# Optimization experiments

Measured on AMD Instinct MI355X. Metric: run time of the kernel, lower is better.

Reference implementation:

```python
import jax, jax.numpy as jnp
import numpy as np

B, S, HID = 2, 2048, 1024
H, KV, D = 8, 4, 128
GROUPS = H // KV
SCALE = D ** -0.5
ROPE_THETA = 10000.0


def _rope_tables(seq_len, dim):
    inv = 1.0 / (ROPE_THETA ** (jnp.arange(0, dim, 2, dtype=jnp.float32) / dim))
    t = jnp.arange(seq_len, dtype=jnp.float32)
    freqs = jnp.outer(t, inv)                          # [S, D/2]
    emb = jnp.concatenate([freqs, freqs], axis=-1)     # [S, D]
    return jnp.cos(emb), jnp.sin(emb)


def _rotate_half(x):
    x1, x2 = jnp.split(x, 2, axis=-1)
    return jnp.concatenate([-x2, x1], axis=-1)


def setup_inputs() -> dict:
    key = jax.random.key(0)
    ks = jax.random.split(key, 7)
    std = 0.02
    hidden = jax.random.normal(ks[0], (B, S, HID), jnp.float32)
    Wq = jax.random.normal(ks[1], (HID, H * D), jnp.float32) * std
    Wk = jax.random.normal(ks[2], (HID, KV * D), jnp.float32) * std
    Wv = jax.random.normal(ks[3], (HID, KV * D), jnp.float32) * std
    Wdt = jax.random.normal(ks[4], (KV * D, H), jnp.float32) * std
    A = jax.random.normal(ks[5], (H,), jnp.float32) * 0.1
    Wo = jax.random.normal(ks[6], (H * D, HID), jnp.float32) * std
    cos, sin = _rope_tables(S, D)
    causal_mask = jnp.triu(jnp.ones((S, S), jnp.int32), 1)[None, None]  # 1 = masked
    return dict(hidden=hidden, Wq=Wq, Wk=Wk, Wv=Wv, Wdt=Wdt, A=A, Wo=Wo,
                cos=cos, sin=sin, causal_mask=causal_mask)


def reference(hidden, Wq, Wk, Wv, Wdt, A, Wo, cos, sin, causal_mask):
    # q/k/v projections -> [B, heads, S, D]
    q = (hidden @ Wq).reshape(B, S, H, D).transpose(0, 2, 1, 3)
    k = (hidden @ Wk).reshape(B, S, KV, D).transpose(0, 2, 1, 3)
    v = (hidden @ Wv).reshape(B, S, KV, D).transpose(0, 2, 1, 3)
    # RoPE
    c = cos[None, None]  # [1,1,S,D]
    s = sin[None, None]
    q = q * c + _rotate_half(q) * s
    k = k * c + _rotate_half(k) * s
    # dynamic mask: dt_proj over flattened per-position value states
    v_flat = v.transpose(0, 2, 1, 3).reshape(B, S, KV * D)
    dt = v_flat @ Wdt                                        # [B, S, H]
    dyn = jnp.exp(A[None, None, :] * jax.nn.softplus(dt))    # [B, S, H]
    attn_bias = dyn.transpose(0, 2, 1)[:, :, None, :]        # [B, H, 1, kv]
    min_val = jnp.finfo(jnp.float32).min
    attn_bias = jnp.where(causal_mask != 0, min_val, attn_bias)  # [B, H, S, S]
    # GQA repeat of kv heads
    k_rep = jnp.repeat(k, GROUPS, axis=1)
    v_rep = jnp.repeat(v, GROUPS, axis=1)
    scores = jnp.einsum('bhqd,bhkd->bhqk', q, k_rep) * SCALE + attn_bias
    w = jax.nn.softmax(scores.astype(jnp.float32), axis=-1).astype(hidden.dtype)
    out = jnp.einsum('bhqk,bhkd->bhqd', w, v_rep)
    out = out.transpose(0, 2, 1, 3).reshape(B, S, H * D)
    return out @ Wo
```

## Files before the change

### kernel.cpp

```cpp
#include <hip/hip_runtime.h>

typedef unsigned short u16;
typedef unsigned int   u32;
typedef __bf16 bf16;
typedef bf16  bf16x8 __attribute__((ext_vector_type(8)));
typedef float f32x4  __attribute__((ext_vector_type(4)));

#define S_LEN 2048
#define SCALE 0.08838834764831845f
#define SMAX  8.0f

__device__ __forceinline__ float bf2f(u16 u) {
  union { u32 i; float f; } v; v.i = ((u32)u) << 16; return v.f;
}
__device__ __forceinline__ u16 f2b(float f) {
  union { float f; u32 i; } v; v.f = f;
  u32 x = v.i;
  u32 r = x + 0x7fffu + ((x >> 16) & 1u);
  return (u16)(r >> 16);
}
__device__ __forceinline__ float2 bfpair(u32 u) {
  union { u32 i; float f; } lo, hi;
  lo.i = u << 16; hi.i = u & 0xffff0000u;
  float2 r; r.x = lo.f; r.y = hi.f; return r;
}

__device__ __forceinline__ void gl_lds16(const u16* g, u16* l) {
  __builtin_amdgcn_global_load_lds(
      (const __attribute__((address_space(1))) void*)g,
      (__attribute__((address_space(3))) void*)l, 16, 0, 0);
}

__device__ __forceinline__ void load16(const float* p, u16* dst) {
  #pragma unroll
  for (int i = 0; i < 16; i += 4) {
    float4 v = *(const float4*)(p + i);
    dst[i]     = f2b(v.x); dst[i + 1] = f2b(v.y);
    dst[i + 2] = f2b(v.z); dst[i + 3] = f2b(v.w);
  }
}

__device__ __forceinline__ void storeo(float* p, float v) { *p = v; }
__device__ __forceinline__ void storeo(u16* p, float v)   { *p = f2b(v); }

__device__ __forceinline__ bf16x8 frag8(const u16* p) {
  union { uint4 u; bf16x8 v; } c;
  c.u = *(const uint4*)p;
  return c.v;
}
__device__ __forceinline__ f32x4 zero4() {
  f32x4 z = {0.f, 0.f, 0.f, 0.f}; return z;
}

__global__ __launch_bounds__(256) void prep_kernel(
    const float* __restrict__ H, u16* __restrict__ HB,
    const float* __restrict__ Wq, const float* __restrict__ Wk,
    const float* __restrict__ Wv, const float* __restrict__ Wo,
    u16* __restrict__ Wqt, u16* __restrict__ Wkt,
    u16* __restrict__ Wvt, u16* __restrict__ Wot)
{
  const int bid = blockIdx.x;
  if (bid < 2048) {
    const size_t base = ((size_t)bid * 256 + threadIdx.x) * 8;
    float4 a = *(const float4*)(H + base);
    float4 b = *(const float4*)(H + base + 4);
    u16 tmp[8];
    tmp[0]=f2b(a.x); tmp[1]=f2b(a.y); tmp[2]=f2b(a.z); tmp[3]=f2b(a.w);
    tmp[4]=f2b(b.x); tmp[5]=f2b(b.y); tmp[6]=f2b(b.z); tmp[7]=f2b(b.w);
    *(uint4*)(HB + base) = *(uint4*)tmp;
    return;
  }
  const int b2 = bid - 2048;
  const float* src; u16* dst; int N, ko, no;
  if (b2 < 256)      { src = Wq; dst = Wqt; N = 1024; int q = b2;       ko = (q >> 4) * 64; no = (q & 15) * 64; }
  else if (b2 < 384) { src = Wk; dst = Wkt; N = 512;  int q = b2 - 256; ko = (q >> 3) * 64; no = (q & 7) * 64; }
  else if (b2 < 512) { src = Wv; dst = Wvt; N = 512;  int q = b2 - 384; ko = (q >> 3) * 64; no = (q & 7) * 64; }
  else               { src = Wo; dst = Wot; N = 1024; int q = b2 - 512; ko = (q >> 4) * 64; no = (q & 15) * 64; }

  __shared__ __align__(16) u16 T[64][68];
  const int t = threadIdx.x;
  const int r = t >> 2, c = (t & 3) * 16;
  {
    u16 tmp[16];
    load16(src + (size_t)(ko + r) * N + no + c, tmp);
    *(uint4*)&T[r][c]     = *(uint4*)tmp;
    *(uint4*)&T[r][c + 8] = *(uint4*)(tmp + 8);
  }
  __syncthreads();
  {
    u16 tmp[16];
    #pragma unroll
    for (int j = 0; j < 16; ++j) tmp[j] = T[c + j][r];
    u16* o = dst + (size_t)(no + r) * 1024 + ko + c;
    *(uint4*)o       = *(uint4*)tmp;
    *(uint4*)(o + 8) = *(uint4*)(tmp + 8);
  }
}

__global__ __launch_bounds__(256) void gemm3(
    const u16* __restrict__ A, int lda, int Kdim,
    const u16* __restrict__ W0, u16* __restrict__ O0, int ldo0,
    const u16* __restrict__ W1, u16* __restrict__ O1, int ldo1,
    const u16* __restrict__ W2, u16* __restrict__ O2, int ldo2,
    int c1, int c2,
    const float* __restrict__ cosb, const float* __restrict__ sinb, int ropeLim)
{
  const int n0 = blockIdx.x * 128;
  const int m0 = blockIdx.y * 128;
  const u16* W; u16* O; int ldo, col;
  if (n0 < c1)      { W = W0; O = O0; ldo = ldo0; col = n0; }
  else if (n0 < c2) { W = W1; O = O1; ldo = ldo1; col = n0 - c1; }
  else              { W = W2; O = O2; ldo = ldo2; col = n0 - c2; }
  const bool doRope = (n0 < ropeLim);

  __shared__ __align__(16) u16 As[128 * 64];
  __shared__ __align__(16) u16 Bs[128 * 64];

  const int t    = threadIdx.x;
  const int w    = t >> 6, lane = t & 63, quad = lane >> 4, l16 = lane & 15;
  const int sw   = l16 & 7;
  const int srow = lane >> 3;
  const int schk = (lane & 7) ^ srow;
  int kcs[2];
  #pragma unroll
  for (int ks = 0; ks < 2; ++ks) kcs[ks] = ((ks * 4 + quad) ^ sw) * 8;

  const u16* Ag = A + (size_t)(m0 + w * 32 + srow) * lda + schk * 8;
  const u16* Bg = W + (size_t)(col + w * 32 + srow) * Kdim + schk * 8;

  f32x4 acc[2][8];
  #pragma unroll
  for (int i2 = 0; i2 < 2; ++i2)
    #pragma unroll
    for (int nt = 0; nt < 8; ++nt) acc[i2][nt] = zero4();

  for (int k0 = 0; k0 < Kdim; k0 += 64) {
    __syncthreads();
    #pragma unroll
    for (int j = 0; j < 4; ++j) {
      gl_lds16(Ag + (size_t)(j * 8) * lda + k0, &As[(w * 4 + j) * 512]);
      gl_lds16(Bg + (size_t)(j * 8) * Kdim + k0, &Bs[(w * 4 + j) * 512]);
    }
    __syncthreads();
    #pragma unroll
    for (int ks = 0; ks < 2; ++ks) {
      bf16x8 a0 = frag8(&As[(w * 32 + l16) * 64 + kcs[ks]]);
      bf16x8 a1 = frag8(&As[(w * 32 + 16 + l16) * 64 + kcs[ks]]);
      #pragma unroll
      for (int nt = 0; nt < 8; ++nt) {
        bf16x8 bw = frag8(&Bs[(nt * 16 + l16) * 64 + kcs[ks]]);
        acc[0][nt] = __builtin_amdgcn_mfma_f32_16x16x32_bf16(a0, bw, acc[0][nt], 0, 0, 0);
        acc[1][nt] = __builtin_amdgcn_mfma_f32_16x16x32_bf16(a1, bw, acc[1][nt], 0, 0, 0);
      }
    }
  }

  if (doRope) {
    #pragma unroll
    for (int i2 = 0; i2 < 2; ++i2)
      #pragma unroll
      for (int r = 0; r < 4; ++r) {
        const int m = m0 + w * 32 + i2 * 16 + quad * 4 + r;
        const int sp_ = m & (S_LEN - 1);
        const float* cp = cosb + (size_t)sp_ * 128;
        const float* sp = sinb + (size_t)sp_ * 128;
        #pragma unroll
        for (int nt = 0; nt < 4; ++nt) {
          const int d = nt * 16 + l16;
          const float a  = acc[i2][nt][r];
          const float bb = acc[i2][nt + 4][r];
          acc[i2][nt][r]     = a * cp[d]       - bb * sp[d];
          acc[i2][nt + 4][r] = bb * cp[d + 64] + a * sp[d + 64];
        }
      }
  }

  #pragma unroll
  for (int i2 = 0; i2 < 2; ++i2)
    #pragma unroll
    for (int nt = 0; nt < 8; ++nt)
      #pragma unroll
      for (int r = 0; r < 4; ++r) {
        const int m = m0 + w * 32 + i2 * 16 + quad * 4 + r;
        const int n = col + nt * 16 + l16;
        O[(size_t)m * ldo + n] = f2b(acc[i2][nt][r]);
      }
}

template <typename TO>
__global__ __launch_bounds__(256) void gemm2(
    const u16* __restrict__ A, int lda, int Kdim,
    const u16* __restrict__ W0, TO* __restrict__ O0, int ldo0,
    const u16* __restrict__ W1, TO* __restrict__ O1, int ldo1,
    const u16* __restrict__ W2, TO* __restrict__ O2, int ldo2,
    int c1, int c2)
{
  const int n0 = blockIdx.x * 64;
  const int m0 = blockIdx.y * 128;
  const u16* W; TO* O; int ldo, col;
  if (n0 < c1)      { W = W0; O = O0; ldo = ldo0; col = n0; }
  else if (n0 < c2) { W = W1; O = O1; ldo = ldo1; col = n0 - c1; }
  else              { W = W2; O = O2; ldo = ldo2; col = n0 - c2; }

  __shared__ __align__(16) u16 As[128 * 64];
  __shared__ __align__(16) u16 Bs[64 * 64];

  const int t    = threadIdx.x;
  const int w    = t >> 6, lane = t & 63, quad = lane >> 4, l16 = lane & 15;
  const int sw   = l16 & 7;
  const int srow = lane >> 3;
  const int schk = (lane & 7) ^ srow;
  int kcs[2];
  #pragma unroll
  for (int ks = 0; ks < 2; ++ks) kcs[ks] = ((ks * 4 + quad) ^ sw) * 8;

  const u16* Ag = A + (size_t)(m0 + w * 32 + srow) * lda + schk * 8;
  const u16* Bg = W + (size_t)(col + w * 16 + srow) * Kdim + schk * 8;

  f32x4 acc[2][4];
  #pragma unroll
  for (int i2 = 0; i2 < 2; ++i2)
    #pragma unroll
    for (int nt = 0; nt < 4; ++nt) acc[i2][nt] = zero4();

  for (int k0 = 0; k0 < Kdim; k0 += 64) {
    __syncthreads();
    #pragma unroll
    for (int j = 0; j < 4; ++j)
      gl_lds16(Ag + (size_t)(j * 8) * lda + k0, &As[(w * 4 + j) * 512]);
    #pragma unroll
    for (int j = 0; j < 2; ++j)
      gl_lds16(Bg + (size_t)(j * 8) * Kdim + k0, &Bs[(w * 2 + j) * 512]);
    __syncthreads();
    #pragma unroll
    for (int ks = 0; ks < 2; ++ks) {
      bf16x8 a0 = frag8(&As[(w * 32 + l16) * 64 + kcs[ks]]);
      bf16x8 a1 = frag8(&As[(w * 32 + 16 + l16) * 64 + kcs[ks]]);
      #pragma unroll
      for (int nt = 0; nt < 4; ++nt) {
        bf16x8 bw = frag8(&Bs[(nt * 16 + l16) * 64 + kcs[ks]]);
        acc[0][nt] = __builtin_amdgcn_mfma_f32_16x16x32_bf16(a0, bw, acc[0][nt], 0, 0, 0);
        acc[1][nt] = __builtin_amdgcn_mfma_f32_16x16x32_bf16(a1, bw, acc[1][nt], 0, 0, 0);
      }
    }
  }
  #pragma unroll
  for (int i2 = 0; i2 < 2; ++i2)
    #pragma unroll
    for (int nt = 0; nt < 4; ++nt)
      #pragma unroll
      for (int r = 0; r < 4; ++r) {
        const int m = m0 + w * 32 + i2 * 16 + quad * 4 + r;
        const int n = col + nt * 16 + l16;
        storeo(O + (size_t)m * ldo + n, acc[i2][nt][r]);
      }
}

__global__ __launch_bounds__(64) void dyn_kernel(const u16* __restrict__ Vb, const float* __restrict__ Wdt,
                                                 const float* __restrict__ Af, float* __restrict__ dynT)
{
  int pos  = blockIdx.x;
  int lane = threadIdx.x;
  float acc[8];
  #pragma unroll
  for (int h = 0; h < 8; ++h) acc[h] = 0.f;
  for (int j = lane; j < 512; j += 64) {
    float v = bf2f(Vb[(size_t)pos * 512 + j]);
    float4 w0 = *(const float4*)(Wdt + j * 8);
    float4 w1 = *(const float4*)(Wdt + j * 8 + 4);
    acc[0] += v * w0.x; acc[1] += v * w0.y; acc[2] += v * w0.z; acc[3] += v * w0.w;
    acc[4] += v * w1.x; acc[5] += v * w1.y; acc[6] += v * w1.z; acc[7] += v * w1.w;
  }
  #pragma unroll
  for (int off = 32; off > 0; off >>= 1)
    #pragma unroll
    for (int h = 0; h < 8; ++h) acc[h] += __shfl_down(acc[h], off, 64);
  if (lane == 0) {
    const int b = pos >> 11, s = pos & (S_LEN - 1);
    #pragma unroll
    for (int h = 0; h < 8; ++h) {
      float dt = acc[h];
      float sp = (dt > 20.f) ? dt : log1pf(__expf(dt));
      dynT[(size_t)(b * 8 + h) * S_LEN + s] = __expf(Af[h] * sp);
    }
  }
}

__global__ __launch_bounds__(256) void vtrans_kernel(const u16* __restrict__ Vb, u16* __restrict__ VTg)
{
  const int sx = blockIdx.x, kvh = blockIdx.y, b = blockIdx.z;
  __shared__ __align__(16) u16 T[64][132];
  const int t = threadIdx.x;
  {
    const int r = t >> 2, c = (t & 3) * 32;
    const u16* src = Vb + (size_t)(b * S_LEN + sx * 64 + r) * 512 + kvh * 128 + c;
    #pragma unroll
    for (int i = 0; i < 4; ++i)
      *(uint4*)&T[r][c + i * 8] = *(const uint4*)(src + i * 8);
  }
  __syncthreads();
  {
    const int d = t >> 1, cs = (t & 1) * 32;
    u16* dst = VTg + ((size_t)((b * 4 + kvh) * 128 + d)) * S_LEN + sx * 64 + cs;
    #pragma unroll
    for (int i = 0; i < 4; ++i) {
      u16 tmp[8];
      #pragma unroll
      for (int j = 0; j < 8; ++j) tmp[j] = T[cs + i * 8 + j][d];
      *(uint4*)(dst + i * 8) = *(uint4*)tmp;
    }
  }
}

__global__ __launch_bounds__(256, 3) void attn_mfma(const u16* __restrict__ Qb, const u16* __restrict__ Kb,
                                                    const u16* __restrict__ VTg, const float* __restrict__ dynT,
                                                    u16* __restrict__ ctx,
                                                    u16* __restrict__ PO, float* __restrict__ PL)
{
  const int idx = blockIdx.x;
  const int g = (idx & 7) | (((idx >> 3) & 1) << 3);
  const int b = g >> 3, h = g & 7, kvh = h >> 1;
  const int fp = 79 - (idx >> 4);
  int s, c;
  if (fp < 8)       { s = fp; c = 0; }
  else if (fp < 24) { s = 8 + ((fp - 8) >> 1);  c = (fp - 8) & 1; }
  else if (fp < 48) { int r2 = fp - 24; int q3 = r2 / 3; s = 16 + q3; c = r2 - q3 * 3; }
  else              { s = 24 + ((fp - 48) >> 2); c = (fp - 48) & 3; }
  const int q0  = s * 64;
  const int kt0 = c * 8;
  const int kt1 = (c == (s >> 3)) ? s : (kt0 + 7);

  __shared__ __align__(16) u16 Ks[64 * 128];
  __shared__ __align__(16) u16 Vs[128 * 64];
  __shared__ __align__(16) u16 Ps[4][16 * 64];

  const int t = threadIdx.x;
  const int wid = t >> 6, lane = t & 63, quad = lane >> 4, l16 = lane & 15;
  const int sw = l16 & 7;

  int kcs[4];
  #pragma unroll
  for (int ks = 0; ks < 4; ++ks) kcs[ks] = ((ks * 4 + quad) ^ sw) * 8;

  const u16* KgL[4];
  const u16* VgL[4];
  #pragma unroll
  for (int j = 0; j < 4; ++j) {
    const int krj = (wid * 4 + j) * 4 + (lane >> 4);
    const int kcj = (lane & 15) ^ (((j & 1) << 2) + (lane >> 4));
    KgL[j] = Kb + (size_t)(b * S_LEN + krj) * 512 + kvh * 128 + kcj * 8;
    const int vrj = (wid * 4 + j) * 8 + (lane >> 3);
    const int vcj = (lane & 7) ^ (lane >> 3);
    VgL[j] = VTg + ((size_t)((b * 4 + kvh) * 128 + vrj)) * S_LEN + vcj * 8;
  }

  bf16x8 qf[4];
  {
    const u16* qrow = Qb + (size_t)(b * S_LEN + q0 + wid * 16 + l16) * 1024 + h * 128 + quad * 8;
    #pragma unroll
    for (int ks = 0; ks < 4; ++ks) qf[ks] = frag8(qrow + ks * 32);
  }

  const float* dynbase = dynT + (size_t)(b * 8 + h) * S_LEN + l16;

  f32x4 accO[8];
  #pragma unroll
  for (int nt = 0; nt < 8; ++nt) accO[nt] = zero4();
  float l_lane[4] = {0.f, 0.f, 0.f, 0.f};

  for (int kt = kt0; kt <= kt1; ++kt) {
    const int k0 = kt * 64;
    __syncthreads();
    #pragma unroll
    for (int j = 0; j < 4; ++j)
      gl_lds16(KgL[j] + (size_t)k0 * 512, &Ks[(wid * 4 + j) * 512]);
    #pragma unroll
    for (int j = 0; j < 4; ++j)
      gl_lds16(VgL[j] + k0, &Vs[(wid * 4 + j) * 512]);
    float dv[4];
    #pragma unroll
    for (int nt = 0; nt < 4; ++nt) dv[nt] = dynbase[k0 + nt * 16];
    __syncthreads();

    f32x4 accS[4];
    #pragma unroll
    for (int nt = 0; nt < 4; ++nt) accS[nt] = zero4();
    __builtin_amdgcn_s_setprio(1);
    #pragma unroll
    for (int ks = 0; ks < 4; ++ks)
      #pragma unroll
      for (int nt = 0; nt < 4; ++nt)
        accS[nt] = __builtin_amdgcn_mfma_f32_16x16x32_bf16(
            qf[ks], frag8(&Ks[(nt * 16 + l16) * 128 + kcs[ks]]), accS[nt], 0, 0, 0);
    __builtin_amdgcn_s_setprio(0);

    if (kt < s) {
      #pragma unroll
      for (int nt = 0; nt < 4; ++nt)
        #pragma unroll
        for (int r = 0; r < 4; ++r) {
          float p = __expf(fmaf(accS[nt][r], SCALE, dv[nt]) - SMAX);
          l_lane[r] += p;
          const int prow = quad * 4 + r;
          Ps[wid][prow * 64 + (((nt * 2 + (l16 >> 3)) ^ (prow & 7)) << 3) + sw] = f2b(p);
        }
    } else {
      const int qq = wid * 16 + quad * 4;
      #pragma unroll
      for (int nt = 0; nt < 4; ++nt) {
        const int kk = nt * 16 + l16;
        #pragma unroll
        for (int r = 0; r < 4; ++r) {
          float p = (kk > qq + r) ? 0.f
                    : __expf(fmaf(accS[nt][r], SCALE, dv[nt]) - SMAX);
          l_lane[r] += p;
          const int prow = quad * 4 + r;
          Ps[wid][prow * 64 + (((nt * 2 + (l16 >> 3)) ^ (prow & 7)) << 3) + sw] = f2b(p);
        }
      }
    }

    __builtin_amdgcn_s_setprio(1);
    #pragma unroll
    for (int ks = 0; ks < 2; ++ks) {
      bf16x8 a = frag8(&Ps[wid][l16 * 64 + kcs[ks]]);
      #pragma unroll
      for (int nt = 0; nt < 8; ++nt)
        accO[nt] = __builtin_amdgcn_mfma_f32_16x16x32_bf16(
            a, frag8(&Vs[(nt * 16 + l16) * 64 + kcs[ks]]), accO[nt], 0, 0, 0);
    }
    __builtin_amdgcn_s_setprio(0);
  }

  #pragma unroll
  for (int off = 1; off < 16; off <<= 1)
    #pragma unroll
    for (int r = 0; r < 4; ++r) l_lane[r] += __shfl_xor(l_lane[r], off, 64);

  if (s < 8) {
    float linv[4];
    #pragma unroll
    for (int r = 0; r < 4; ++r) linv[r] = 1.f / l_lane[r];
    #pragma unroll
    for (int nt = 0; nt < 8; ++nt)
      #pragma unroll
      for (int r = 0; r < 4; ++r) {
        const int qq = q0 + wid * 16 + quad * 4 + r;
        const int d  = nt * 16 + l16;
        ctx[(size_t)(b * S_LEN + qq) * 1024 + h * 128 + d] = f2b(accO[nt][r] * linv[r]);
      }
  } else {
    const int slot = g * 72 + (fp - 8);
    u16 tmp[32];
    #pragma unroll
    for (int nt = 0; nt < 8; ++nt)
      #pragma unroll
      for (int r = 0; r < 4; ++r) tmp[nt * 4 + r] = f2b(accO[nt][r]);
    u16* po = PO + (size_t)slot * 8192 + wid * 2048 + lane * 32;
    #pragma unroll
    for (int i = 0; i < 4; ++i) *(uint4*)(po + i * 8) = *(uint4*)(tmp + i * 8);
    if (l16 == 0) {
      #pragma unroll
      for (int r = 0; r < 4; ++r) PL[slot * 64 + wid * 16 + quad * 4 + r] = l_lane[r];
    }
  }
}

__global__ __launch_bounds__(64) void attn_combine(const u16* __restrict__ PO, const float* __restrict__ PL,
                                                   u16* __restrict__ ctx)
{
  const int s = 8 + (int)blockIdx.x;
  const int g = (int)blockIdx.y;
  const int b = g >> 3, h = g & 7;
  const int g2 = s >> 3;
  const int nch = g2 + 1;
  const int base = (g2 == 1) ? 8 : (g2 == 2) ? 24 : 48;
  const int slot0 = g * 72 + base + (s - g2 * 8) * nch - 8;
  const int lane = threadIdx.x, quad = lane >> 4, l16 = lane & 15;

  for (int wid = 0; wid < 4; ++wid) {
    float acc[32];
    #pragma unroll
    for (int i = 0; i < 32; ++i) acc[i] = 0.f;
    float ls[4] = {0.f, 0.f, 0.f, 0.f};

    for (int cth = 0; cth < nch; ++cth) {
      const u16* po = PO + (size_t)(slot0 + cth) * 8192 + wid * 2048 + lane * 32;
      #pragma unroll
      for (int i = 0; i < 4; ++i) {
        uint4 v = *(const uint4*)(po + i * 8);
        u32 u[4] = {v.x, v.y, v.z, v.w};
        #pragma unroll
        for (int j = 0; j < 4; ++j) {
          float2 p = bfpair(u[j]);
          acc[i * 8 + 2 * j]     += p.x;
          acc[i * 8 + 2 * j + 1] += p.y;
        }
      }
      #pragma unroll
      for (int r = 0; r < 4; ++r) ls[r] += PL[(slot0 + cth) * 64 + wid * 16 + quad * 4 + r];
    }

    float linv[4];
    #pragma unroll
    for (int r = 0; r < 4; ++r) linv[r] = 1.f / ls[r];
    #pragma unroll
    for (int nt = 0; nt < 8; ++nt)
      #pragma unroll
      for (int r = 0; r < 4; ++r) {
        const int qq = s * 64 + wid * 16 + quad * 4 + r;
        const int d  = nt * 16 + l16;
        ctx[(size_t)(b * S_LEN + qq) * 1024 + h * 128 + d] = f2b(acc[nt * 4 + r] * linv[r]);
      }
  }
}

extern "C" void kernel_launch(void* const* d_in, const int* in_sizes, int n_in,
                              void* d_out, int out_size, void* d_ws, size_t ws_size,
                              hipStream_t stream)
{
  const float* hidden = (const float*)d_in[0];
  const float* Wq     = (const float*)d_in[1];
  const float* Wk     = (const float*)d_in[2];
  const float* Wv     = (const float*)d_in[3];
  const float* Wdt    = (const float*)d_in[4];
  const float* Af     = (const float*)d_in[5];
  const float* Wo     = (const float*)d_in[6];
  const float* cosb   = (const float*)d_in[7];
  const float* sinb   = (const float*)d_in[8];
  float* out = (float*)d_out;

  u16* Qb  = (u16*)d_ws;
  u16* Kb  = Qb + (size_t)4096 * 1024;
  u16* Vb  = Kb + (size_t)4096 * 512;
  u16* VTg = Vb + (size_t)4096 * 512;
  float* dynT = (float*)(VTg + (size_t)4096 * 512);
  u16* PO = (u16*)(dynT + (size_t)16 * S_LEN);
  float* PL = (float*)(PO + (size_t)16 * 72 * 8192);
  u16* HB  = (u16*)(PL + (size_t)16 * 72 * 64);
  u16* Wqt = HB  + (size_t)4096 * 1024;
  u16* Wkt = Wqt + (size_t)1024 * 1024;
  u16* Wvt = Wkt + (size_t)512 * 1024;
  u16* Wot = Wvt + (size_t)512 * 1024;
  u16* ctx = Qb;

  prep_kernel<<<2816, 256, 0, stream>>>(hidden, HB, Wq, Wk, Wv, Wo, Wqt, Wkt, Wvt, Wot);
  gemm3<<<dim3(16, 32), 256, 0, stream>>>(HB, 1024, 1024,
      Wqt, Qb, 1024,
      Wkt, Kb,  512,
      Wvt, Vb,  512,
      1024, 1536,
      cosb, sinb, 1536);
  dyn_kernel<<<4096, 64, 0, stream>>>(Vb, Wdt, Af, dynT);
  vtrans_kernel<<<dim3(32, 4, 2), 256, 0, stream>>>(Vb, VTg);
  attn_mfma<<<1280, 256, 0, stream>>>(Qb, Kb, VTg, dynT, ctx, PO, PL);
  attn_combine<<<dim3(24, 16), 64, 0, stream>>>(PO, PL, ctx);
  gemm2<float><<<dim3(16, 32), 256, 0, stream>>>(ctx, 1024, 1024,
      Wot, out, 1024,
      Wot, out, 1024,
      Wot, out, 1024,
      1 << 30, 1 << 30);
}
```

Baseline: 220.9 us.

## Double-buffer K/V tiles in attention, fix P swizzle, widen dyn and combine kernels

```diff
diff --git a/kernel.cpp b/kernel.cpp
--- a/kernel.cpp
+++ b/kernel.cpp
@@ -256,18 +256,25 @@
       }
 }
 
-__global__ __launch_bounds__(64) void dyn_kernel(const u16* __restrict__ Vb, const float* __restrict__ Wdt,
-                                                 const float* __restrict__ Af, float* __restrict__ dynT)
-{
-  int pos  = blockIdx.x;
-  int lane = threadIdx.x;
+__global__ __launch_bounds__(256) void dyn_kernel(const u16* __restrict__ Vb, const float* __restrict__ Wdt,
+                                                  const float* __restrict__ Af, float* __restrict__ dynT)
+{
+  __shared__ __align__(16) float Wl[4096];
+  const int t = threadIdx.x;
+  #pragma unroll
+  for (int i = 0; i < 4; ++i)
+    *(float4*)&Wl[(t + i * 256) * 4] = *(const float4*)(Wdt + (t + i * 256) * 4);
+  __syncthreads();
+
+  const int wid = t >> 6, lane = t & 63;
+  const int pos = blockIdx.x * 4 + wid;
   float acc[8];
   #pragma unroll
   for (int h = 0; h < 8; ++h) acc[h] = 0.f;
   for (int j = lane; j < 512; j += 64) {
     float v = bf2f(Vb[(size_t)pos * 512 + j]);
-    float4 w0 = *(const float4*)(Wdt + j * 8);
-    float4 w1 = *(const float4*)(Wdt + j * 8 + 4);
+    float4 w0 = *(const float4*)&Wl[j * 8];
+    float4 w1 = *(const float4*)&Wl[j * 8 + 4];
     acc[0] += v * w0.x; acc[1] += v * w0.y; acc[2] += v * w0.z; acc[3] += v * w0.w;
     acc[4] += v * w1.x; acc[5] += v * w1.y; acc[6] += v * w1.z; acc[7] += v * w1.w;
   }
@@ -312,7 +319,7 @@
   }
 }
 
-__global__ __launch_bounds__(256, 3) void attn_mfma(const u16* __restrict__ Qb, const u16* __restrict__ Kb,
+__global__ __launch_bounds__(256, 2) void attn_mfma(const u16* __restrict__ Qb, const u16* __restrict__ Kb,
                                                     const u16* __restrict__ VTg, const float* __restrict__ dynT,
                                                     u16* __restrict__ ctx,
                                                     u16* __restrict__ PO, float* __restrict__ PL)
@@ -330,17 +337,20 @@
   const int kt0 = c * 8;
   const int kt1 = (c == (s >> 3)) ? s : (kt0 + 7);
 
-  __shared__ __align__(16) u16 Ks[64 * 128];
-  __shared__ __align__(16) u16 Vs[128 * 64];
+  __shared__ __align__(16) u16 Ks[2][64 * 128];
+  __shared__ __align__(16) u16 Vs[2][128 * 64];
   __shared__ __align__(16) u16 Ps[4][16 * 64];
 
   const int t = threadIdx.x;
   const int wid = t >> 6, lane = t & 63, quad = lane >> 4, l16 = lane & 15;
   const int sw = l16 & 7;
 
-  int kcs[4];
+  int kcs[4], pcs[2];
   #pragma unroll
   for (int ks = 0; ks < 4; ++ks) kcs[ks] = ((ks * 4 + quad) ^ sw) * 8;
+  const int fr = ((l16 >> 2) << 1) | (l16 & 1);
+  #pragma unroll
+  for (int ks = 0; ks < 2; ++ks) pcs[ks] = ((ks * 4 + quad) ^ fr) * 8;
 
   const u16* KgL[4];
   const u16* VgL[4];
@@ -368,19 +378,35 @@
   for (int nt = 0; nt < 8; ++nt) accO[nt] = zero4();
   float l_lane[4] = {0.f, 0.f, 0.f, 0.f};
 
+  {
+    const int k0p = kt0 * 64;
+    const int bp = kt0 & 1;
+    #pragma unroll
+    for (int j = 0; j < 4; ++j)
+      gl_lds16(KgL[j] + (size_t)k0p * 512, &Ks[bp][(wid * 4 + j) * 512]);
+    #pragma unroll
+    for (int j = 0; j < 4; ++j)
+      gl_lds16(VgL[j] + k0p, &Vs[bp][(wid * 4 + j) * 512]);
+  }
+
   for (int kt = kt0; kt <= kt1; ++kt) {
     const int k0 = kt * 64;
-    __syncthreads();
-    #pragma unroll
-    for (int j = 0; j < 4; ++j)
-      gl_lds16(KgL[j] + (size_t)k0 * 512, &Ks[(wid * 4 + j) * 512]);
-    #pragma unroll
-    for (int j = 0; j < 4; ++j)
-      gl_lds16(VgL[j] + k0, &Vs[(wid * 4 + j) * 512]);
     float dv[4];
     #pragma unroll
     for (int nt = 0; nt < 4; ++nt) dv[nt] = dynbase[k0 + nt * 16];
     __syncthreads();
+    if (kt < kt1) {
+      const int k0n = k0 + 64;
+      const int nb = (kt + 1) & 1;
+      #pragma unroll
+      for (int j = 0; j < 4; ++j)
+        gl_lds16(KgL[j] + (size_t)k0n * 512, &Ks[nb][(wid * 4 + j) * 512]);
+      #pragma unroll
+      for (int j = 0; j < 4; ++j)
+        gl_lds16(VgL[j] + k0n, &Vs[nb][(wid * 4 + j) * 512]);
+    }
+    const u16* ksb = Ks[kt & 1];
+    const u16* vsb = Vs[kt & 1];
 
     f32x4 accS[4];
     #pragma unroll
@@ -391,7 +417,7 @@
       #pragma unroll
       for (int nt = 0; nt < 4; ++nt)
         accS[nt] = __builtin_amdgcn_mfma_f32_16x16x32_bf16(
-            qf[ks], frag8(&Ks[(nt * 16 + l16) * 128 + kcs[ks]]), accS[nt], 0, 0, 0);
+            qf[ks], frag8(&ksb[(nt * 16 + l16) * 128 + kcs[ks]]), accS[nt], 0, 0, 0);
     __builtin_amdgcn_s_setprio(0);
 
     if (kt < s) {
@@ -402,7 +428,8 @@
           float p = __expf(fmaf(accS[nt][r], SCALE, dv[nt]) - SMAX);
           l_lane[r] += p;
           const int prow = quad * 4 + r;
-          Ps[wid][prow * 64 + (((nt * 2 + (l16 >> 3)) ^ (prow & 7)) << 3) + sw] = f2b(p);
+          const int fw = (quad << 1) | (r & 1);
+          Ps[wid][prow * 64 + (((nt * 2 + (l16 >> 3)) ^ fw) << 3) + sw] = f2b(p);
         }
     } else {
       const int qq = wid * 16 + quad * 4;
@@ -415,7 +442,8 @@
                     : __expf(fmaf(accS[nt][r], SCALE, dv[nt]) - SMAX);
           l_lane[r] += p;
           const int prow = quad * 4 + r;
-          Ps[wid][prow * 64 + (((nt * 2 + (l16 >> 3)) ^ (prow & 7)) << 3) + sw] = f2b(p);
+          const int fw = (quad << 1) | (r & 1);
+          Ps[wid][prow * 64 + (((nt * 2 + (l16 >> 3)) ^ fw) << 3) + sw] = f2b(p);
         }
       }
     }
@@ -423,11 +451,11 @@
     __builtin_amdgcn_s_setprio(1);
     #pragma unroll
     for (int ks = 0; ks < 2; ++ks) {
-      bf16x8 a = frag8(&Ps[wid][l16 * 64 + kcs[ks]]);
+      bf16x8 a = frag8(&Ps[wid][l16 * 64 + pcs[ks]]);
       #pragma unroll
       for (int nt = 0; nt < 8; ++nt)
         accO[nt] = __builtin_amdgcn_mfma_f32_16x16x32_bf16(
-            a, frag8(&Vs[(nt * 16 + l16) * 64 + kcs[ks]]), accO[nt], 0, 0, 0);
+            a, frag8(&vsb[(nt * 16 + l16) * 64 + kcs[ks]]), accO[nt], 0, 0, 0);
     }
     __builtin_amdgcn_s_setprio(0);
   }
@@ -466,8 +494,8 @@
   }
 }
 
-__global__ __launch_bounds__(64) void attn_combine(const u16* __restrict__ PO, const float* __restrict__ PL,
-                                                   u16* __restrict__ ctx)
+__global__ __launch_bounds__(256) void attn_combine(const u16* __restrict__ PO, const float* __restrict__ PL,
+                                                    u16* __restrict__ ctx)
 {
   const int s = 8 + (int)blockIdx.x;
   const int g = (int)blockIdx.y;
@@ -476,43 +504,42 @@
   const int nch = g2 + 1;
   const int base = (g2 == 1) ? 8 : (g2 == 2) ? 24 : 48;
   const int slot0 = g * 72 + base + (s - g2 * 8) * nch - 8;
-  const int lane = threadIdx.x, quad = lane >> 4, l16 = lane & 15;
-
-  for (int wid = 0; wid < 4; ++wid) {
-    float acc[32];
-    #pragma unroll
-    for (int i = 0; i < 32; ++i) acc[i] = 0.f;
-    float ls[4] = {0.f, 0.f, 0.f, 0.f};
-
-    for (int cth = 0; cth < nch; ++cth) {
-      const u16* po = PO + (size_t)(slot0 + cth) * 8192 + wid * 2048 + lane * 32;
-      #pragma unroll
-      for (int i = 0; i < 4; ++i) {
-        uint4 v = *(const uint4*)(po + i * 8);
-        u32 u[4] = {v.x, v.y, v.z, v.w};
-        #pragma unroll
-        for (int j = 0; j < 4; ++j) {
-          float2 p = bfpair(u[j]);
-          acc[i * 8 + 2 * j]     += p.x;
-          acc[i * 8 + 2 * j + 1] += p.y;
-        }
-      }
-      #pragma unroll
-      for (int r = 0; r < 4; ++r) ls[r] += PL[(slot0 + cth) * 64 + wid * 16 + quad * 4 + r];
-    }
-
-    float linv[4];
-    #pragma unroll
-    for (int r = 0; r < 4; ++r) linv[r] = 1.f / ls[r];
-    #pragma unroll
-    for (int nt = 0; nt < 8; ++nt)
-      #pragma unroll
-      for (int r = 0; r < 4; ++r) {
-        const int qq = s * 64 + wid * 16 + quad * 4 + r;
-        const int d  = nt * 16 + l16;
-        ctx[(size_t)(b * S_LEN + qq) * 1024 + h * 128 + d] = f2b(acc[nt * 4 + r] * linv[r]);
-      }
-  }
+  const int t = threadIdx.x;
+  const int wid = t >> 6, lane = t & 63, quad = lane >> 4, l16 = lane & 15;
+
+  float acc[32];
+  #pragma unroll
+  for (int i = 0; i < 32; ++i) acc[i] = 0.f;
+  float ls[4] = {0.f, 0.f, 0.f, 0.f};
+
+  for (int cth = 0; cth < nch; ++cth) {
+    const u16* po = PO + (size_t)(slot0 + cth) * 8192 + wid * 2048 + lane * 32;
+    #pragma unroll
+    for (int i = 0; i < 4; ++i) {
+      uint4 v = *(const uint4*)(po + i * 8);
+      u32 u[4] = {v.x, v.y, v.z, v.w};
+      #pragma unroll
+      for (int j = 0; j < 4; ++j) {
+        float2 p = bfpair(u[j]);
+        acc[i * 8 + 2 * j]     += p.x;
+        acc[i * 8 + 2 * j + 1] += p.y;
+      }
+    }
+    #pragma unroll
+    for (int r = 0; r < 4; ++r) ls[r] += PL[(slot0 + cth) * 64 + wid * 16 + quad * 4 + r];
+  }
+
+  float linv[4];
+  #pragma unroll
+  for (int r = 0; r < 4; ++r) linv[r] = 1.f / ls[r];
+  #pragma unroll
+  for (int nt = 0; nt < 8; ++nt)
+    #pragma unroll
+    for (int r = 0; r < 4; ++r) {
+      const int qq = s * 64 + wid * 16 + quad * 4 + r;
+      const int d  = nt * 16 + l16;
+      ctx[(size_t)(b * S_LEN + qq) * 1024 + h * 128 + d] = f2b(acc[nt * 4 + r] * linv[r]);
+    }
 }
 
 extern "C" void kernel_launch(void* const* d_in, const int* in_sizes, int n_in,
@@ -551,10 +578,10 @@
       Wvt, Vb,  512,
       1024, 1536,
       cosb, sinb, 1536);
-  dyn_kernel<<<4096, 64, 0, stream>>>(Vb, Wdt, Af, dynT);
+  dyn_kernel<<<1024, 256, 0, stream>>>(Vb, Wdt, Af, dynT);
   vtrans_kernel<<<dim3(32, 4, 2), 256, 0, stream>>>(Vb, VTg);
   attn_mfma<<<1280, 256, 0, stream>>>(Qb, Kb, VTg, dynT, ctx, PO, PL);
-  attn_combine<<<dim3(24, 16), 64, 0, stream>>>(PO, PL, ctx);
+  attn_combine<<<dim3(24, 16), 256, 0, stream>>>(PO, PL, ctx);
   gemm2<float><<<dim3(16, 32), 256, 0, stream>>>(ctx, 1024, 1024,
       Wot, out, 1024,
       Wot, out, 1024,
```

Result: no change. 221.1 us (+0.0%).
